# Kernel tuning notes

Hardware: AMD Instinct MI355X
Metric: run time of the kernel (lower is better)

The kernel has to match this reference:

```python
import jax, jax.numpy as jnp
import numpy as np


def setup_inputs() -> dict:
    key = jax.random.key(0)
    ks = jax.random.split(key, 8)
    B, C, T, V = 64, 256, 64, 25
    h = 8
    x_cls = jax.random.normal(ks[0], (B, C, 1, V), dtype=jnp.float32)
    x_patch = jax.random.normal(ks[1], (B, C, T, V), dtype=jnp.float32)
    s = 0.02
    q_w = jax.random.normal(ks[2], (C, C), dtype=jnp.float32) * s
    k_w = jax.random.normal(ks[3], (C, C), dtype=jnp.float32) * s
    v_w = jax.random.normal(ks[4], (C, C), dtype=jnp.float32) * s
    temp = jnp.ones((h, 1), dtype=jnp.float32)
    proj_w = jax.random.normal(ks[5], (C, C), dtype=jnp.float32) * s
    proj_b = jnp.zeros((C,), dtype=jnp.float32)
    return {"x_cls": x_cls, "x_patch": x_patch, "q_w": q_w, "k_w": k_w,
            "v_w": v_w, "temp": temp, "proj_w": proj_w, "proj_b": proj_b}


def reference(x_cls, x_patch, q_w, k_w, v_w, temp, proj_w, proj_b):
    B, C, _, V = x_cls.shape
    T = x_patch.shape[2]
    h = temp.shape[0]
    hd = C // h
    # (B, C, 1, V) -> (B, V, C) token layout; patches -> (B, T*V, C)
    xc = jnp.transpose(x_cls.reshape(B, C, V), (0, 2, 1))
    xp = jnp.transpose(x_patch.reshape(B, C, T * V), (0, 2, 1))
    # nn.Linear: y = x @ W.T (no bias since qkv_bias=False)
    q = (xc @ q_w.T).reshape(B, V, h, hd).transpose(0, 2, 1, 3)        # (B,h,V,hd)
    k = (xp @ k_w.T).reshape(B, T * V, h, hd).transpose(0, 2, 1, 3)    # (B,h,TV,hd)
    v = (xp @ v_w.T).reshape(B, T * V, h, hd).transpose(0, 2, 1, 3)    # (B,h,TV,hd)
    # scores: (B,h,V,TV), scaled by 1/sqrt(hd) then per-head temperature
    scale = 1.0 / jnp.sqrt(jnp.asarray(hd, dtype=q.dtype))
    attn = jnp.einsum('bhqd,bhkd->bhqk', q, k) * scale
    attn = attn * temp[None, :, :, None]  # temp (h,1) -> broadcast (1,h,1,1)
    attn = jax.nn.softmax(attn, axis=-1)
    out = jnp.einsum('bhqk,bhkd->bhqd', attn, v)                       # (B,h,V,hd)
    out = out.transpose(0, 2, 1, 3).reshape(B, V, C)
    out = out @ proj_w.T + proj_b
    return jnp.transpose(out, (0, 2, 1)).reshape(B, C, 1, V)
```

## Files before the change

### kernel.cpp

```cpp
#include <hip/hip_runtime.h>

#define B_ 64
#define C_ 256
#define TV_ 1600
#define V_ 25
#define H_ 8

typedef __attribute__((ext_vector_type(2))) int   intx2;
typedef __attribute__((ext_vector_type(4))) int   intx4;
typedef __attribute__((ext_vector_type(2))) float floatx2;
typedef __attribute__((ext_vector_type(4))) float floatx4;
typedef __attribute__((ext_vector_type(8))) short short8;

__device__ __forceinline__ unsigned short f2bf(float f) {
    union { float f; unsigned u; } c; c.f = f;
    unsigned u = c.u;
    u += 0x7fffu + ((u >> 16) & 1u);
    return (unsigned short)(u >> 16);
}
__device__ __forceinline__ int pk_bf2(float a, float b) {
    return (int)((unsigned)f2bf(a) | ((unsigned)f2bf(b) << 16));
}

__global__ __launch_bounds__(256) void k_pre(
        const float* __restrict__ xcls, const float* __restrict__ qw,
        const float* __restrict__ kw, const float* __restrict__ temp,
        unsigned short* __restrict__ QT,
        const float* __restrict__ vw, const float* __restrict__ pw,
        unsigned short* __restrict__ VWB, unsigned short* __restrict__ PWB) {
    __shared__ float smem[9152];
    const int blk = blockIdx.x;
    const int t = threadIdx.x;

    if (blk < 512) {
        float* xq  = smem;
        float* kws = smem;
        float* qh  = smem + 8320;
        const int b = blk >> 3, h = blk & 7;
        {
            const float* src = xcls + ((size_t)(b * C_ + t)) * V_;
            #pragma unroll
            for (int q = 0; q < V_; q++) xq[q * 260 + t] = src[q];
        }
        __syncthreads();
        floatx4 kreg[8];
        {
            const float* krow = kw + (size_t)(h * 32 + (t >> 3)) * C_ + (t & 7) * 32;
            #pragma unroll
            for (int j = 0; j < 8; j++) kreg[j] = *(const floatx4*)(krow + 4 * j);
        }
        for (int idx = t; idx < 800; idx += 256) {
            const int q = idx >> 5, d = idx & 31;
            const float* qwr = qw + (size_t)(h * 32 + d) * C_;
            float acc = 0.f;
            #pragma unroll 4
            for (int c4 = 0; c4 < 64; c4++) {
                const floatx4 a = *(const floatx4*)(qwr + 4 * c4);
                const floatx4 x = *(const floatx4*)&xq[q * 260 + 4 * c4];
                acc += a[0] * x[0] + a[1] * x[1] + a[2] * x[2] + a[3] * x[3];
            }
            qh[q * 33 + d] = acc;
        }
        __syncthreads();
        {
            float* kdst = kws + (t >> 3) * 260 + (t & 7) * 32;
            #pragma unroll
            for (int j = 0; j < 8; j++) *(floatx4*)(kdst + 4 * j) = kreg[j];
        }
        __syncthreads();
        const float scale = temp[h] * 0.17677669529663689f * 1.4426950408889634f;
        const int qp = t & 31, cg = t >> 5;
        const int c0 = cg * 32;
        if (qp < 25) {
            floatx4 a4[8];
            #pragma unroll
            for (int j = 0; j < 8; j++) a4[j] = (floatx4){0.f, 0.f, 0.f, 0.f};
            for (int d = 0; d < 32; d++) {
                const float a = qh[qp * 33 + d];
                #pragma unroll
                for (int j4 = 0; j4 < 8; j4++) {
                    const floatx4 k4 = *(const floatx4*)&kws[d * 260 + c0 + 4 * j4];
                    a4[j4][0] += a * k4[0]; a4[j4][1] += a * k4[1];
                    a4[j4][2] += a * k4[2]; a4[j4][3] += a * k4[3];
                }
            }
            unsigned short* dst = QT + ((size_t)((b * H_ + h) * 25 + qp)) * C_ + c0;
            #pragma unroll
            for (int j8 = 0; j8 < 4; j8++) {
                intx4 w;
                w[0] = pk_bf2(scale * a4[j8 * 2][0],     scale * a4[j8 * 2][1]);
                w[1] = pk_bf2(scale * a4[j8 * 2][2],     scale * a4[j8 * 2][3]);
                w[2] = pk_bf2(scale * a4[j8 * 2 + 1][0], scale * a4[j8 * 2 + 1][1]);
                w[3] = pk_bf2(scale * a4[j8 * 2 + 1][2], scale * a4[j8 * 2 + 1][3]);
                *(intx4*)(dst + j8 * 8) = w;
            }
        }
    } else {
        const int g = (blk - 512) * 256 + t;
        const floatx4 v = ((const floatx4*)vw)[g];
        const floatx4 p = ((const floatx4*)pw)[g];
        ((intx2*)VWB)[g] = (intx2){pk_bf2(v[0], v[1]), pk_bf2(v[2], v[3])};
        ((intx2*)PWB)[g] = (intx2){pk_bf2(p[0], p[1]), pk_bf2(p[2], p[3])};
    }
}

__global__ __launch_bounds__(512, 2) void k2_attn(
        const float* __restrict__ xp, const unsigned short* __restrict__ QT,
        const unsigned short* __restrict__ VWB, float* __restrict__ OAP,
        float* __restrict__ LP) {
    __shared__ unsigned short Xs[2][8192];
    __shared__ unsigned short Ps[8][32 * 40];
    __shared__ unsigned short Vs[8][32 * 40];

    const int blk = blockIdx.x;
    const int b = blk & 63, s = blk >> 6;
    const int tid = threadIdx.x;
    const int h = tid >> 6;
    const int lane = tid & 63;
    const int quad = lane >> 4, l16 = lane & 15;

    const float* xrow = xp + (size_t)b * C_ * TV_ + (size_t)((tid >> 4) * 8) * TV_
                      + s * 160 + (tid & 15) * 2;

    short8 qf[2][8];
    {
        const unsigned short* qb = QT + (size_t)(b * H_ + h) * 25 * C_;
        #pragma unroll
        for (int mt = 0; mt < 2; mt++)
            #pragma unroll
            for (int ks = 0; ks < 8; ks++)
                qf[mt][ks] = *(const short8*)(qb + (mt * 16 + l16) * C_ + ks * 32 + quad * 8);
    }
    short8 vwf[2][8];
    #pragma unroll
    for (int dt = 0; dt < 2; dt++)
        #pragma unroll
        for (int ks = 0; ks < 8; ks++)
            vwf[dt][ks] = *(const short8*)(VWB + (size_t)(h * 32 + dt * 16 + l16) * C_ + ks * 32 + quad * 8);

    floatx4 oc[2][2];
    #pragma unroll
    for (int mt = 0; mt < 2; mt++)
        #pragma unroll
        for (int dt = 0; dt < 2; dt++) oc[mt][dt] = (floatx4){0.f, 0.f, 0.f, 0.f};
    float lsum[2][4];
    #pragma unroll
    for (int mt = 0; mt < 2; mt++)
        #pragma unroll
        for (int r = 0; r < 4; r++) lsum[mt][r] = 0.f;

    floatx2 pf[8];
    #pragma unroll
    for (int j = 0; j < 8; j++) pf[j] = *(const floatx2*)(xrow + (size_t)j * TV_);
    {
        intx4 w0, w1;
        w0[0] = pk_bf2(pf[0][0], pf[1][0]); w0[1] = pk_bf2(pf[2][0], pf[3][0]);
        w0[2] = pk_bf2(pf[4][0], pf[5][0]); w0[3] = pk_bf2(pf[6][0], pf[7][0]);
        w1[0] = pk_bf2(pf[0][1], pf[1][1]); w1[1] = pk_bf2(pf[2][1], pf[3][1]);
        w1[2] = pk_bf2(pf[4][1], pf[5][1]); w1[3] = pk_bf2(pf[6][1], pf[7][1]);
        *(intx4*)&Xs[0][(tid * 2 + 0) * 8] = w0;
        *(intx4*)&Xs[0][(tid * 2 + 1) * 8] = w1;
    }
    __syncthreads();

    for (int ti = 0; ti < 5; ti++) {
        const int cur = ti & 1;
        if (ti < 4) {
            #pragma unroll
            for (int j = 0; j < 8; j++)
                pf[j] = *(const floatx2*)(xrow + (ti + 1) * 32 + (size_t)j * TV_);
        }
        const unsigned short* xsc = Xs[cur];
        floatx4 sc[2][2], va[2][2];
        #pragma unroll
        for (int i = 0; i < 2; i++)
            #pragma unroll
            for (int j = 0; j < 2; j++) {
                sc[i][j] = (floatx4){0.f, 0.f, 0.f, 0.f};
                va[i][j] = (floatx4){0.f, 0.f, 0.f, 0.f};
            }
        #pragma unroll
        for (int ks = 0; ks < 8; ks++) {
            const short8 xf0 = *(const short8*)&xsc[(((ks * 4 + quad) * 32) + l16) * 8];
            const short8 xf1 = *(const short8*)&xsc[(((ks * 4 + quad) * 32) + 16 + l16) * 8];
            sc[0][0] = __builtin_amdgcn_mfma_f32_16x16x32_bf16(qf[0][ks], xf0, sc[0][0], 0, 0, 0);
            sc[0][1] = __builtin_amdgcn_mfma_f32_16x16x32_bf16(qf[0][ks], xf1, sc[0][1], 0, 0, 0);
            sc[1][0] = __builtin_amdgcn_mfma_f32_16x16x32_bf16(qf[1][ks], xf0, sc[1][0], 0, 0, 0);
            sc[1][1] = __builtin_amdgcn_mfma_f32_16x16x32_bf16(qf[1][ks], xf1, sc[1][1], 0, 0, 0);
            va[0][0] = __builtin_amdgcn_mfma_f32_16x16x32_bf16(xf0, vwf[0][ks], va[0][0], 0, 0, 0);
            va[0][1] = __builtin_amdgcn_mfma_f32_16x16x32_bf16(xf0, vwf[1][ks], va[0][1], 0, 0, 0);
            va[1][0] = __builtin_amdgcn_mfma_f32_16x16x32_bf16(xf1, vwf[0][ks], va[1][0], 0, 0, 0);
            va[1][1] = __builtin_amdgcn_mfma_f32_16x16x32_bf16(xf1, vwf[1][ks], va[1][1], 0, 0, 0);
        }
        #pragma unroll
        for (int mt = 0; mt < 2; mt++)
            #pragma unroll
            for (int g = 0; g < 2; g++)
                #pragma unroll
                for (int r = 0; r < 4; r++) {
                    const float p = __builtin_amdgcn_exp2f(sc[mt][g][r]);
                    lsum[mt][r] += p;
                    Ps[h][(mt * 16 + quad * 4 + r) * 40 + g * 16 + l16] = f2bf(p);
                }
        #pragma unroll
        for (int g = 0; g < 2; g++)
            #pragma unroll
            for (int dt = 0; dt < 2; dt++)
                *(intx2*)&Vs[h][(dt * 16 + l16) * 40 + g * 16 + quad * 4] =
                    (intx2){pk_bf2(va[g][dt][0], va[g][dt][1]),
                            pk_bf2(va[g][dt][2], va[g][dt][3])};
        #pragma unroll
        for (int mt = 0; mt < 2; mt++) {
            const short8 pa = *(const short8*)&Ps[h][(mt * 16 + l16) * 40 + quad * 8];
            #pragma unroll
            for (int dt = 0; dt < 2; dt++) {
                const short8 vb = *(const short8*)&Vs[h][(dt * 16 + l16) * 40 + quad * 8];
                oc[mt][dt] = __builtin_amdgcn_mfma_f32_16x16x32_bf16(pa, vb, oc[mt][dt], 0, 0, 0);
            }
        }
        if (ti < 4) {
            intx4 w0, w1;
            w0[0] = pk_bf2(pf[0][0], pf[1][0]); w0[1] = pk_bf2(pf[2][0], pf[3][0]);
            w0[2] = pk_bf2(pf[4][0], pf[5][0]); w0[3] = pk_bf2(pf[6][0], pf[7][0]);
            w1[0] = pk_bf2(pf[0][1], pf[1][1]); w1[1] = pk_bf2(pf[2][1], pf[3][1]);
            w1[2] = pk_bf2(pf[4][1], pf[5][1]); w1[3] = pk_bf2(pf[6][1], pf[7][1]);
            *(intx4*)&Xs[cur ^ 1][(tid * 2 + 0) * 8] = w0;
            *(intx4*)&Xs[cur ^ 1][(tid * 2 + 1) * 8] = w1;
        }
        __syncthreads();
    }
    #pragma unroll
    for (int mt = 0; mt < 2; mt++)
        #pragma unroll
        for (int r = 0; r < 4; r++) {
            float v = lsum[mt][r];
            #pragma unroll
            for (int off = 1; off < 16; off <<= 1) v += __shfl_xor(v, off, 64);
            lsum[mt][r] = v;
        }
    const size_t bh = (size_t)(b * H_ + h);
    if (l16 == 0) {
        #pragma unroll
        for (int mt = 0; mt < 2; mt++)
            #pragma unroll
            for (int r = 0; r < 4; r++) {
                const int q = mt * 16 + quad * 4 + r;
                LP[bh * 320 + s * 32 + q] = lsum[mt][r];
            }
    }
    #pragma unroll
    for (int mt = 0; mt < 2; mt++)
        #pragma unroll
        for (int dt = 0; dt < 2; dt++)
            #pragma unroll
            for (int r = 0; r < 4; r++) {
                const int q = mt * 16 + quad * 4 + r;
                if (q < 25)
                    OAP[((size_t)(bh * 25 + q)) * 320 + s * 32 + dt * 16 + l16] = oc[mt][dt][r];
            }
}

__global__ __launch_bounds__(256) void k3_proj(const float* __restrict__ OAP,
        const float* __restrict__ LP, const unsigned short* __restrict__ PWB,
        const float* __restrict__ pb, float* __restrict__ y) {
    __shared__ unsigned short OB[32 * 264];
    __shared__ float rl_s[256];
    const int blk = blockIdx.x;
    const int b = blk & 63, i0 = (blk >> 6) * 64;
    const int t = threadIdx.x;
    const int wv = t >> 6, lane = t & 63;
    const int quad = lane >> 4, l16 = lane & 15;
    {
        const int h = t >> 5, q = t & 31;
        const float* lp = LP + (size_t)(b * H_ + h) * 320 + q;
        float lv = 0.f;
        #pragma unroll
        for (int s = 0; s < 10; s++) lv += lp[s * 32];
        rl_s[t] = (q < 25) ? 1.0f / lv : 0.0f;
    }
    __syncthreads();
    for (int idx = t; idx < 8192; idx += 256) {
        const int q = idx >> 8, j = idx & 255;
        const int h2 = j >> 5, d = j & 31;
        float val = 0.f;
        if (q < 25) {
            const float* op = OAP + ((size_t)(b * H_ + h2) * 25 + q) * 320 + d;
            float acc = 0.f;
            #pragma unroll
            for (int s = 0; s < 10; s++) acc += op[s * 32];
            val = acc * rl_s[h2 * 32 + q];
        }
        OB[q * 264 + j] = f2bf(val);
    }
    __syncthreads();
    floatx4 oc[2];
    oc[0] = (floatx4){0.f, 0.f, 0.f, 0.f};
    oc[1] = (floatx4){0.f, 0.f, 0.f, 0.f};
    const int i = i0 + wv * 16 + l16;
    #pragma unroll
    for (int ks = 0; ks < 8; ks++) {
        const short8 a0 = *(const short8*)&OB[l16 * 264 + ks * 32 + quad * 8];
        const short8 a1 = *(const short8*)&OB[(16 + l16) * 264 + ks * 32 + quad * 8];
        const short8 bv = *(const short8*)(PWB + (size_t)i * C_ + ks * 32 + quad * 8);
        oc[0] = __builtin_amdgcn_mfma_f32_16x16x32_bf16(a0, bv, oc[0], 0, 0, 0);
        oc[1] = __builtin_amdgcn_mfma_f32_16x16x32_bf16(a1, bv, oc[1], 0, 0, 0);
    }
    const float bias = pb[i];
    #pragma unroll
    for (int mt = 0; mt < 2; mt++)
        #pragma unroll
        for (int r = 0; r < 4; r++) {
            const int q = mt * 16 + quad * 4 + r;
            if (q < 25) y[(size_t)b * 6400 + i * 25 + q] = oc[mt][r] + bias;
        }
}

extern "C" void kernel_launch(void* const* d_in, const int* in_sizes, int n_in,
                              void* d_out, int out_size, void* d_ws, size_t ws_size,
                              hipStream_t stream) {
    const float* xcls = (const float*)d_in[0];
    const float* xp   = (const float*)d_in[1];
    const float* qw   = (const float*)d_in[2];
    const float* kw   = (const float*)d_in[3];
    const float* vw   = (const float*)d_in[4];
    const float* temp = (const float*)d_in[5];
    const float* pw   = (const float*)d_in[6];
    const float* pb   = (const float*)d_in[7];
    float* y = (float*)d_out;

    if (ws_size < (size_t)23863296) return;
    char* ws = (char*)d_ws;
    unsigned short* QT  = (unsigned short*)ws;
    float*          OAP = (float*)(ws + 6561792);
    float*          LP  = (float*)(ws + 22945792);
    unsigned short* VWB = (unsigned short*)(ws + 23601152);
    unsigned short* PWB = (unsigned short*)(ws + 23732224);

    hipLaunchKernelGGL(k_pre,   dim3(576), dim3(256), 0, stream,
                       xcls, qw, kw, temp, QT, vw, pw, VWB, PWB);
    hipLaunchKernelGGL(k2_attn, dim3(640), dim3(512), 0, stream, xp, QT, VWB, OAP, LP);
    hipLaunchKernelGGL(k3_proj, dim3(256), dim3(256), 0, stream, OAP, LP, PWB, pb, y);
}
```

Measured before the change: 269.4 us.

## Warp-specialize attention into score and value-projection wave groups with pipelined PV

Splits each attention block into two 512-thread wave groups: one computes QK scores, exp and row sums, and the other computes the V projection and the P·V accumulation one tile behind, using double-buffered P and V tiles in LDS. Blocks grow to 1024 threads and cover twice as many tokens (10 tiles of 32), which halves the grid and halves the partial buffers that the projection kernel reduces. The aim is to overlap score and value MFMA work across waves and to lower per-wave register pressure. In exchange there are more block-wide barriers per tile, the grid is smaller at 320 blocks, and occupancy now depends on the 1024-thread launch bound.

```diff
diff --git a/kernel.cpp b/kernel.cpp
--- a/kernel.cpp
+++ b/kernel.cpp
@@ -5,10 +5,10 @@
 #define TV_ 1600
 #define V_ 25
 #define H_ 8
+#define NT_ 10
 
 typedef __attribute__((ext_vector_type(2))) int   intx2;
 typedef __attribute__((ext_vector_type(4))) int   intx4;
-typedef __attribute__((ext_vector_type(2))) float floatx2;
 typedef __attribute__((ext_vector_type(4))) float floatx4;
 typedef __attribute__((ext_vector_type(8))) short short8;
 
@@ -104,160 +104,189 @@
     }
 }
 
-__global__ __launch_bounds__(512, 2) void k2_attn(
+__global__ __launch_bounds__(1024, 4) void k2_attn(
         const float* __restrict__ xp, const unsigned short* __restrict__ QT,
         const unsigned short* __restrict__ VWB, float* __restrict__ OAP,
         float* __restrict__ LP) {
     __shared__ unsigned short Xs[2][8192];
-    __shared__ unsigned short Ps[8][32 * 40];
-    __shared__ unsigned short Vs[8][32 * 40];
+    __shared__ unsigned short Ps[2][8][32*40];
+    __shared__ unsigned short Vs[2][8][32*40];
 
     const int blk = blockIdx.x;
     const int b = blk & 63, s = blk >> 6;
     const int tid = threadIdx.x;
-    const int h = tid >> 6;
+    const int wv = tid >> 6;
+    const int h = wv & 7;
+    const int role = wv >> 3;
     const int lane = tid & 63;
     const int quad = lane >> 4, l16 = lane & 15;
 
-    const float* xrow = xp + (size_t)b * C_ * TV_ + (size_t)((tid >> 4) * 8) * TV_
-                      + s * 160 + (tid & 15) * 2;
-
-    short8 qf[2][8];
-    {
-        const unsigned short* qb = QT + (size_t)(b * H_ + h) * 25 * C_;
+    const int cg = tid >> 5, n32 = tid & 31;
+    const float* xrow = xp + (size_t)b * C_ * TV_ + (size_t)(cg * 8) * TV_
+                      + s * 320 + n32;
+    const size_t bh = (size_t)(b * H_ + h);
+
+    if (role == 0) {
+        short8 qf[2][8];
+        {
+            const unsigned short* qb = QT + bh * 25 * C_;
+            #pragma unroll
+            for (int mt = 0; mt < 2; mt++)
+                #pragma unroll
+                for (int ks = 0; ks < 8; ks++)
+                    qf[mt][ks] = *(const short8*)(qb + (mt * 16 + l16) * C_ + ks * 32 + quad * 8);
+        }
+        float lsum[2][4];
         #pragma unroll
         for (int mt = 0; mt < 2; mt++)
             #pragma unroll
+            for (int r = 0; r < 4; r++) lsum[mt][r] = 0.f;
+
+        float f[8];
+        #pragma unroll
+        for (int j = 0; j < 8; j++) f[j] = xrow[(size_t)j * TV_];
+        *(intx4*)&Xs[0][tid * 8] = (intx4){pk_bf2(f[0], f[1]), pk_bf2(f[2], f[3]),
+                                           pk_bf2(f[4], f[5]), pk_bf2(f[6], f[7])};
+        __syncthreads();
+
+        for (int ti = 0; ti < NT_; ti++) {
+            const int cur = ti & 1;
+            if (ti < NT_ - 1) {
+                #pragma unroll
+                for (int j = 0; j < 8; j++) f[j] = xrow[(ti + 1) * 32 + (size_t)j * TV_];
+            }
+            floatx4 sc[2][2];
+            #pragma unroll
+            for (int i = 0; i < 2; i++)
+                #pragma unroll
+                for (int g = 0; g < 2; g++) sc[i][g] = (floatx4){0.f, 0.f, 0.f, 0.f};
+            #pragma unroll
+            for (int ks = 0; ks < 8; ks++) {
+                const short8 xf0 = *(const short8*)&Xs[cur][(((ks * 4 + quad) * 32) + l16) * 8];
+                const short8 xf1 = *(const short8*)&Xs[cur][(((ks * 4 + quad) * 32) + 16 + l16) * 8];
+                sc[0][0] = __builtin_amdgcn_mfma_f32_16x16x32_bf16(qf[0][ks], xf0, sc[0][0], 0, 0, 0);
+                sc[0][1] = __builtin_amdgcn_mfma_f32_16x16x32_bf16(qf[0][ks], xf1, sc[0][1], 0, 0, 0);
+                sc[1][0] = __builtin_amdgcn_mfma_f32_16x16x32_bf16(qf[1][ks], xf0, sc[1][0], 0, 0, 0);
+                sc[1][1] = __builtin_amdgcn_mfma_f32_16x16x32_bf16(qf[1][ks], xf1, sc[1][1], 0, 0, 0);
+            }
+            #pragma unroll
+            for (int mt = 0; mt < 2; mt++)
+                #pragma unroll
+                for (int g = 0; g < 2; g++)
+                    #pragma unroll
+                    for (int r = 0; r < 4; r++) {
+                        const float p = __builtin_amdgcn_exp2f(sc[mt][g][r]);
+                        lsum[mt][r] += p;
+                        Ps[cur][h][(mt * 16 + quad * 4 + r) * 40 + g * 16 + l16] = f2bf(p);
+                    }
+            if (ti < NT_ - 1)
+                *(intx4*)&Xs[cur ^ 1][tid * 8] = (intx4){pk_bf2(f[0], f[1]), pk_bf2(f[2], f[3]),
+                                                         pk_bf2(f[4], f[5]), pk_bf2(f[6], f[7])};
+            __syncthreads();
+        }
+        #pragma unroll
+        for (int mt = 0; mt < 2; mt++)
+            #pragma unroll
+            for (int r = 0; r < 4; r++) {
+                float v = lsum[mt][r];
+                #pragma unroll
+                for (int off = 1; off < 16; off <<= 1) v += __shfl_xor(v, off, 64);
+                lsum[mt][r] = v;
+            }
+        if (l16 == 0) {
+            #pragma unroll
+            for (int mt = 0; mt < 2; mt++)
+                #pragma unroll
+                for (int r = 0; r < 4; r++) {
+                    const int q = mt * 16 + quad * 4 + r;
+                    LP[bh * 160 + s * 32 + q] = lsum[mt][r];
+                }
+        }
+    } else {
+        short8 vwf[2][8];
+        #pragma unroll
+        for (int dt = 0; dt < 2; dt++)
+            #pragma unroll
             for (int ks = 0; ks < 8; ks++)
-                qf[mt][ks] = *(const short8*)(qb + (mt * 16 + l16) * C_ + ks * 32 + quad * 8);
-    }
-    short8 vwf[2][8];
-    #pragma unroll
-    for (int dt = 0; dt < 2; dt++)
-        #pragma unroll
-        for (int ks = 0; ks < 8; ks++)
-            vwf[dt][ks] = *(const short8*)(VWB + (size_t)(h * 32 + dt * 16 + l16) * C_ + ks * 32 + quad * 8);
-
-    floatx4 oc[2][2];
-    #pragma unroll
-    for (int mt = 0; mt < 2; mt++)
-        #pragma unroll
-        for (int dt = 0; dt < 2; dt++) oc[mt][dt] = (floatx4){0.f, 0.f, 0.f, 0.f};
-    float lsum[2][4];
-    #pragma unroll
-    for (int mt = 0; mt < 2; mt++)
-        #pragma unroll
-        for (int r = 0; r < 4; r++) lsum[mt][r] = 0.f;
-
-    floatx2 pf[8];
-    #pragma unroll
-    for (int j = 0; j < 8; j++) pf[j] = *(const floatx2*)(xrow + (size_t)j * TV_);
-    {
-        intx4 w0, w1;
-        w0[0] = pk_bf2(pf[0][0], pf[1][0]); w0[1] = pk_bf2(pf[2][0], pf[3][0]);
-        w0[2] = pk_bf2(pf[4][0], pf[5][0]); w0[3] = pk_bf2(pf[6][0], pf[7][0]);
-        w1[0] = pk_bf2(pf[0][1], pf[1][1]); w1[1] = pk_bf2(pf[2][1], pf[3][1]);
-        w1[2] = pk_bf2(pf[4][1], pf[5][1]); w1[3] = pk_bf2(pf[6][1], pf[7][1]);
-        *(intx4*)&Xs[0][(tid * 2 + 0) * 8] = w0;
-        *(intx4*)&Xs[0][(tid * 2 + 1) * 8] = w1;
-    }
-    __syncthreads();
-
-    for (int ti = 0; ti < 5; ti++) {
-        const int cur = ti & 1;
-        if (ti < 4) {
-            #pragma unroll
-            for (int j = 0; j < 8; j++)
-                pf[j] = *(const floatx2*)(xrow + (ti + 1) * 32 + (size_t)j * TV_);
-        }
-        const unsigned short* xsc = Xs[cur];
-        floatx4 sc[2][2], va[2][2];
-        #pragma unroll
-        for (int i = 0; i < 2; i++)
-            #pragma unroll
-            for (int j = 0; j < 2; j++) {
-                sc[i][j] = (floatx4){0.f, 0.f, 0.f, 0.f};
-                va[i][j] = (floatx4){0.f, 0.f, 0.f, 0.f};
-            }
-        #pragma unroll
-        for (int ks = 0; ks < 8; ks++) {
-            const short8 xf0 = *(const short8*)&xsc[(((ks * 4 + quad) * 32) + l16) * 8];
-            const short8 xf1 = *(const short8*)&xsc[(((ks * 4 + quad) * 32) + 16 + l16) * 8];
-            sc[0][0] = __builtin_amdgcn_mfma_f32_16x16x32_bf16(qf[0][ks], xf0, sc[0][0], 0, 0, 0);
-            sc[0][1] = __builtin_amdgcn_mfma_f32_16x16x32_bf16(qf[0][ks], xf1, sc[0][1], 0, 0, 0);
-            sc[1][0] = __builtin_amdgcn_mfma_f32_16x16x32_bf16(qf[1][ks], xf0, sc[1][0], 0, 0, 0);
-            sc[1][1] = __builtin_amdgcn_mfma_f32_16x16x32_bf16(qf[1][ks], xf1, sc[1][1], 0, 0, 0);
-            va[0][0] = __builtin_amdgcn_mfma_f32_16x16x32_bf16(xf0, vwf[0][ks], va[0][0], 0, 0, 0);
-            va[0][1] = __builtin_amdgcn_mfma_f32_16x16x32_bf16(xf0, vwf[1][ks], va[0][1], 0, 0, 0);
-            va[1][0] = __builtin_amdgcn_mfma_f32_16x16x32_bf16(xf1, vwf[0][ks], va[1][0], 0, 0, 0);
-            va[1][1] = __builtin_amdgcn_mfma_f32_16x16x32_bf16(xf1, vwf[1][ks], va[1][1], 0, 0, 0);
-        }
+                vwf[dt][ks] = *(const short8*)(VWB + (size_t)(h * 32 + dt * 16 + l16) * C_ + ks * 32 + quad * 8);
+        floatx4 oc[2][2];
         #pragma unroll
         for (int mt = 0; mt < 2; mt++)
             #pragma unroll
+            for (int dt = 0; dt < 2; dt++) oc[mt][dt] = (floatx4){0.f, 0.f, 0.f, 0.f};
+
+        float f[8];
+        #pragma unroll
+        for (int j = 0; j < 8; j++) f[j] = xrow[(size_t)j * TV_];
+        *(intx4*)&Xs[0][tid * 8] = (intx4){pk_bf2(f[0], f[1]), pk_bf2(f[2], f[3]),
+                                           pk_bf2(f[4], f[5]), pk_bf2(f[6], f[7])};
+        __syncthreads();
+
+        for (int ti = 0; ti < NT_; ti++) {
+            const int cur = ti & 1;
+            if (ti < NT_ - 1) {
+                #pragma unroll
+                for (int j = 0; j < 8; j++) f[j] = xrow[(ti + 1) * 32 + (size_t)j * TV_];
+            }
+            if (ti > 0) {
+                #pragma unroll
+                for (int mt = 0; mt < 2; mt++) {
+                    const short8 pa = *(const short8*)&Ps[cur ^ 1][h][(mt * 16 + l16) * 40 + quad * 8];
+                    #pragma unroll
+                    for (int dt = 0; dt < 2; dt++) {
+                        const short8 vb = *(const short8*)&Vs[cur ^ 1][h][(dt * 16 + l16) * 40 + quad * 8];
+                        oc[mt][dt] = __builtin_amdgcn_mfma_f32_16x16x32_bf16(pa, vb, oc[mt][dt], 0, 0, 0);
+                    }
+                }
+            }
+            floatx4 va[2][2];
+            #pragma unroll
             for (int g = 0; g < 2; g++)
                 #pragma unroll
+                for (int dt = 0; dt < 2; dt++) va[g][dt] = (floatx4){0.f, 0.f, 0.f, 0.f};
+            #pragma unroll
+            for (int ks = 0; ks < 8; ks++) {
+                const short8 xf0 = *(const short8*)&Xs[cur][(((ks * 4 + quad) * 32) + l16) * 8];
+                const short8 xf1 = *(const short8*)&Xs[cur][(((ks * 4 + quad) * 32) + 16 + l16) * 8];
+                va[0][0] = __builtin_amdgcn_mfma_f32_16x16x32_bf16(xf0, vwf[0][ks], va[0][0], 0, 0, 0);
+                va[0][1] = __builtin_amdgcn_mfma_f32_16x16x32_bf16(xf0, vwf[1][ks], va[0][1], 0, 0, 0);
+                va[1][0] = __builtin_amdgcn_mfma_f32_16x16x32_bf16(xf1, vwf[0][ks], va[1][0], 0, 0, 0);
+                va[1][1] = __builtin_amdgcn_mfma_f32_16x16x32_bf16(xf1, vwf[1][ks], va[1][1], 0, 0, 0);
+            }
+            #pragma unroll
+            for (int g = 0; g < 2; g++)
+                #pragma unroll
+                for (int dt = 0; dt < 2; dt++)
+                    *(intx2*)&Vs[cur][h][(dt * 16 + l16) * 40 + g * 16 + quad * 4] =
+                        (intx2){pk_bf2(va[g][dt][0], va[g][dt][1]),
+                                pk_bf2(va[g][dt][2], va[g][dt][3])};
+            if (ti < NT_ - 1)
+                *(intx4*)&Xs[cur ^ 1][tid * 8] = (intx4){pk_bf2(f[0], f[1]), pk_bf2(f[2], f[3]),
+                                                         pk_bf2(f[4], f[5]), pk_bf2(f[6], f[7])};
+            __syncthreads();
+        }
+        {
+            #pragma unroll
+            for (int mt = 0; mt < 2; mt++) {
+                const short8 pa = *(const short8*)&Ps[1][h][(mt * 16 + l16) * 40 + quad * 8];
+                #pragma unroll
+                for (int dt = 0; dt < 2; dt++) {
+                    const short8 vb = *(const short8*)&Vs[1][h][(dt * 16 + l16) * 40 + quad * 8];
+                    oc[mt][dt] = __builtin_amdgcn_mfma_f32_16x16x32_bf16(pa, vb, oc[mt][dt], 0, 0, 0);
+                }
+            }
+        }
+        #pragma unroll
+        for (int mt = 0; mt < 2; mt++)
+            #pragma unroll
+            for (int dt = 0; dt < 2; dt++)
+                #pragma unroll
                 for (int r = 0; r < 4; r++) {
-                    const float p = __builtin_amdgcn_exp2f(sc[mt][g][r]);
-                    lsum[mt][r] += p;
-                    Ps[h][(mt * 16 + quad * 4 + r) * 40 + g * 16 + l16] = f2bf(p);
-                }
-        #pragma unroll
-        for (int g = 0; g < 2; g++)
-            #pragma unroll
-            for (int dt = 0; dt < 2; dt++)
-                *(intx2*)&Vs[h][(dt * 16 + l16) * 40 + g * 16 + quad * 4] =
-                    (intx2){pk_bf2(va[g][dt][0], va[g][dt][1]),
-                            pk_bf2(va[g][dt][2], va[g][dt][3])};
-        #pragma unroll
-        for (int mt = 0; mt < 2; mt++) {
-            const short8 pa = *(const short8*)&Ps[h][(mt * 16 + l16) * 40 + quad * 8];
-            #pragma unroll
-            for (int dt = 0; dt < 2; dt++) {
-                const short8 vb = *(const short8*)&Vs[h][(dt * 16 + l16) * 40 + quad * 8];
-                oc[mt][dt] = __builtin_amdgcn_mfma_f32_16x16x32_bf16(pa, vb, oc[mt][dt], 0, 0, 0);
-            }
-        }
-        if (ti < 4) {
-            intx4 w0, w1;
-            w0[0] = pk_bf2(pf[0][0], pf[1][0]); w0[1] = pk_bf2(pf[2][0], pf[3][0]);
-            w0[2] = pk_bf2(pf[4][0], pf[5][0]); w0[3] = pk_bf2(pf[6][0], pf[7][0]);
-            w1[0] = pk_bf2(pf[0][1], pf[1][1]); w1[1] = pk_bf2(pf[2][1], pf[3][1]);
-            w1[2] = pk_bf2(pf[4][1], pf[5][1]); w1[3] = pk_bf2(pf[6][1], pf[7][1]);
-            *(intx4*)&Xs[cur ^ 1][(tid * 2 + 0) * 8] = w0;
-            *(intx4*)&Xs[cur ^ 1][(tid * 2 + 1) * 8] = w1;
-        }
-        __syncthreads();
-    }
-    #pragma unroll
-    for (int mt = 0; mt < 2; mt++)
-        #pragma unroll
-        for (int r = 0; r < 4; r++) {
-            float v = lsum[mt][r];
-            #pragma unroll
-            for (int off = 1; off < 16; off <<= 1) v += __shfl_xor(v, off, 64);
-            lsum[mt][r] = v;
-        }
-    const size_t bh = (size_t)(b * H_ + h);
-    if (l16 == 0) {
-        #pragma unroll
-        for (int mt = 0; mt < 2; mt++)
-            #pragma unroll
-            for (int r = 0; r < 4; r++) {
-                const int q = mt * 16 + quad * 4 + r;
-                LP[bh * 320 + s * 32 + q] = lsum[mt][r];
-            }
-    }
-    #pragma unroll
-    for (int mt = 0; mt < 2; mt++)
-        #pragma unroll
-        for (int dt = 0; dt < 2; dt++)
-            #pragma unroll
-            for (int r = 0; r < 4; r++) {
-                const int q = mt * 16 + quad * 4 + r;
-                if (q < 25)
-                    OAP[((size_t)(bh * 25 + q)) * 320 + s * 32 + dt * 16 + l16] = oc[mt][dt][r];
-            }
+                    const int q = mt * 16 + quad * 4 + r;
+                    if (q < 25)
+                        OAP[((size_t)(bh * 25 + q)) * 160 + s * 32 + dt * 16 + l16] = oc[mt][dt][r];
+                }
+    }
 }
 
 __global__ __launch_bounds__(256) void k3_proj(const float* __restrict__ OAP,
@@ -272,10 +301,10 @@
     const int quad = lane >> 4, l16 = lane & 15;
     {
         const int h = t >> 5, q = t & 31;
-        const float* lp = LP + (size_t)(b * H_ + h) * 320 + q;
+        const float* lp = LP + (size_t)(b * H_ + h) * 160 + q;
         float lv = 0.f;
         #pragma unroll
-        for (int s = 0; s < 10; s++) lv += lp[s * 32];
+        for (int s = 0; s < 5; s++) lv += lp[s * 32];
         rl_s[t] = (q < 25) ? 1.0f / lv : 0.0f;
     }
     __syncthreads();
@@ -284,10 +313,10 @@
         const int h2 = j >> 5, d = j & 31;
         float val = 0.f;
         if (q < 25) {
-            const float* op = OAP + ((size_t)(b * H_ + h2) * 25 + q) * 320 + d;
+            const float* op = OAP + ((size_t)(b * H_ + h2) * 25 + q) * 160 + d;
             float acc = 0.f;
             #pragma unroll
-            for (int s = 0; s < 10; s++) acc += op[s * 32];
+            for (int s = 0; s < 5; s++) acc += op[s * 32];
             val = acc * rl_s[h2 * 32 + q];
         }
         OB[q * 264 + j] = f2bf(val);
@@ -328,16 +357,16 @@
     const float* pb   = (const float*)d_in[7];
     float* y = (float*)d_out;
 
-    if (ws_size < (size_t)23863296) return;
+    if (ws_size < (size_t)15343616) return;
     char* ws = (char*)d_ws;
     unsigned short* QT  = (unsigned short*)ws;
     float*          OAP = (float*)(ws + 6561792);
-    float*          LP  = (float*)(ws + 22945792);
-    unsigned short* VWB = (unsigned short*)(ws + 23601152);
-    unsigned short* PWB = (unsigned short*)(ws + 23732224);
-
-    hipLaunchKernelGGL(k_pre,   dim3(576), dim3(256), 0, stream,
+    float*          LP  = (float*)(ws + 14753792);
+    unsigned short* VWB = (unsigned short*)(ws + 15081472);
+    unsigned short* PWB = (unsigned short*)(ws + 15212544);
+
+    hipLaunchKernelGGL(k_pre,   dim3(576), dim3(256),  0, stream,
                        xcls, qw, kw, temp, QT, vw, pw, VWB, PWB);
-    hipLaunchKernelGGL(k2_attn, dim3(640), dim3(512), 0, stream, xp, QT, VWB, OAP, LP);
-    hipLaunchKernelGGL(k3_proj, dim3(256), dim3(256), 0, stream, OAP, LP, PWB, pb, y);
-}
+    hipLaunchKernelGGL(k2_attn, dim3(320), dim3(1024), 0, stream, xp, QT, VWB, OAP, LP);
+    hipLaunchKernelGGL(k3_proj, dim3(256), dim3(256),  0, stream, OAP, LP, PWB, pb, y);
+}
```

Measured after the change: 269.3 us. About the same (-0.1%).
